# Kernel tuning notes

Measured on AMD Instinct MI355X. Metric: run time of the kernel, lower is better.

Reference implementation:

```python
import jax, jax.numpy as jnp
import numpy as np

D = 512      # model_dim
H = 8        # num_heads
HD = D // H  # head_dim = 64
S = 196      # tokens per channel (14x14 grid)
CHANNELS = np.array([2, 4, 6, 4], dtype=np.int32)  # multiplex channels per sample


def setup_inputs() -> dict:
    key = jax.random.key(0)
    ks = jax.random.split(key, 8)
    C = int(CHANNELS.sum())  # 16
    n = lambda k, shp, s=1.0: jax.random.normal(k, shp, dtype=jnp.float32) * s
    return {
        "x_query": n(ks[0], (C, S, D)),
        "x_keyval": n(ks[1], (C, S, D)),
        "pos": n(ks[2], (C, S, D)),
        "channels": CHANNELS,
        "Wq": n(ks[3], (D, D), 0.02), "bq": jnp.zeros((D,), jnp.float32),
        "Wk": n(ks[4], (D, D), 0.02), "bk": jnp.zeros((D,), jnp.float32),
        "Wv": n(ks[5], (D, D), 0.02), "bv": jnp.zeros((D,), jnp.float32),
        "Wo": n(ks[6], (D, D), 0.02), "bo": jnp.zeros((D,), jnp.float32),
    }


def reference(x_query, x_keyval, pos, channels, Wq, bq, Wk, bk, Wv, bv, Wo, bo):
    C, S_, D_ = x_query.shape
    ch = np.asarray(channels)
    # segment id per packed token; segment i has length channels[i]*S (== cu_seq_len blocks)
    seg = np.repeat(np.arange(ch.shape[0]), ch * S_)                # [T] static
    block_mask = seg[:, None] == seg[None, :]                        # [T,T] static bool

    xq = x_query.reshape(-1, D_)   # [T,D]
    xk = x_keyval.reshape(-1, D_)
    p = pos.reshape(-1, D_)

    # positional embedding fused into Q/K before projection (query_pos/key_pos)
    q = ((xq + p) @ Wq + bq).reshape(-1, H, HD)
    k = ((xk + p) @ Wk + bk).reshape(-1, H, HD)
    v = (xk @ Wv + bv).reshape(-1, H, HD)

    scale = 1.0 / np.sqrt(HD)
    scores = jnp.einsum('qhd,khd->hqk', q, k) * scale               # [H,T,T]
    scores = jnp.where(block_mask[None], scores, jnp.float32(-1e30))
    attn = jax.nn.softmax(scores, axis=-1)
    out = jnp.einsum('hqk,khd->qhd', attn, v).reshape(-1, D_)       # [T,D]
    out = out @ Wo + bo
    return out.reshape(C, S_, D_)
```

## Files before the change

### kernel.cpp

```cpp
#include <hip/hip_runtime.h>


typedef short short8 __attribute__((ext_vector_type(8)));
typedef float f32x4 __attribute__((ext_vector_type(4)));

__device__ __forceinline__ float b2f(unsigned short u) {
    union { float f; unsigned int i; } x; x.i = ((unsigned int)u) << 16; return x.f;
}
__device__ __forceinline__ unsigned short f2b(float f) {
    union { float f; unsigned int i; } x; x.f = f;
    unsigned int r = x.i + 0x7fffu + ((x.i >> 16) & 1u);
    return (unsigned short)(r >> 16);
}

#define NE 1605632
#define WE 262144
#define GS 72

__launch_bounds__(256)
__global__ void prep(const float* __restrict__ xq, const float* __restrict__ xk,
                     const float* __restrict__ pos,
                     const float* __restrict__ W0, const float* __restrict__ W1,
                     const float* __restrict__ W2, const float* __restrict__ W3,
                     unsigned short* __restrict__ WF,
                     unsigned short* __restrict__ aqb, unsigned short* __restrict__ akb,
                     unsigned short* __restrict__ xkbb) {
    const int tid = threadIdx.x;
    if (blockIdx.z < 4) {
        if (blockIdx.x >= 128) return;
        const float* W = blockIdx.z == 0 ? W0 : blockIdx.z == 1 ? W1 : blockIdx.z == 2 ? W2 : W3;
        unsigned short* T = WF + (size_t)blockIdx.z * WE;
        const int s = blockIdx.x * 4 + (tid >> 6);
        const int f = s >> 4, t = s & 15;
        const int lane = tid & 63, quad = lane >> 4, l16 = lane & 15;
        short8 o;
        #pragma unroll
        for (int j = 0; j < 8; ++j)
            o[j] = (short)f2b(W[(size_t)(t * 32 + quad * 8 + j) * 512 + f * 16 + l16]);
        *(short8*)(T + (size_t)s * 512 + lane * 8) = o;
    } else {
        const size_t e = ((size_t)blockIdx.x * 256 + tid) * 8;
        f32x4 q0 = *(const f32x4*)(xq + e),  q1 = *(const f32x4*)(xq + e + 4);
        f32x4 k0 = *(const f32x4*)(xk + e),  k1 = *(const f32x4*)(xk + e + 4);
        f32x4 p0 = *(const f32x4*)(pos + e), p1 = *(const f32x4*)(pos + e + 4);
        short8 a, b, c;
        #pragma unroll
        for (int j = 0; j < 4; ++j) {
            a[j] = (short)f2b(q0[j] + p0[j]); a[4 + j] = (short)f2b(q1[j] + p1[j]);
            b[j] = (short)f2b(k0[j] + p0[j]); b[4 + j] = (short)f2b(k1[j] + p1[j]);
            c[j] = (short)f2b(k0[j]);         c[4 + j] = (short)f2b(k1[j]);
        }
        *(short8*)(aqb + e)  = a;
        *(short8*)(akb + e)  = b;
        *(short8*)(xkbb + e) = c;
    }
}

template <bool OUT_F32>
__device__ __forceinline__ void gemm_wave(const unsigned short* __restrict__ A,
                                          const unsigned short* __restrict__ WFw,
                                          const float* __restrict__ bias,
                                          void* __restrict__ C,
                                          int m0, int n0) {
    const int lane = threadIdx.x & 63;
    const int quad = lane >> 4, l16 = lane & 15;
    const int f0 = n0 >> 4;
    const unsigned short* Arow = A + (size_t)(m0 + l16) * 512 + quad * 8;
    const unsigned short* Bbase = WFw + (size_t)lane * 8;

    f32x4 acc[4] = {};
    #pragma unroll 4
    for (int t = 0; t < 16; ++t) {
        short8 af = *(const short8*)(Arow + t * 32);
        #pragma unroll
        for (int nt = 0; nt < 4; ++nt) {
            short8 bf = *(const short8*)(Bbase + (size_t)((f0 + nt) * 16 + t) * 512);
            acc[nt] = __builtin_amdgcn_mfma_f32_16x16x32_bf16(af, bf, acc[nt], 0, 0, 0);
        }
    }
    #pragma unroll
    for (int nt = 0; nt < 4; ++nt) {
        const int col = n0 + nt * 16 + l16;
        const float bv = bias[col];
        #pragma unroll
        for (int r = 0; r < 4; ++r) {
            const int row = m0 + quad * 4 + r;
            float cv = acc[nt][r] + bv;
            if constexpr (OUT_F32) ((float*)C)[(size_t)row * 512 + col] = cv;
            else ((unsigned short*)C)[(size_t)row * 512 + col] = f2b(cv);
        }
    }
}

__launch_bounds__(256)
__global__ void qkv_gemm(const unsigned short* __restrict__ aqb,
                         const unsigned short* __restrict__ akb,
                         const unsigned short* __restrict__ xkbb,
                         const unsigned short* __restrict__ WF,
                         const float* __restrict__ bq, const float* __restrict__ bk,
                         const float* __restrict__ bv,
                         unsigned short* __restrict__ qb, unsigned short* __restrict__ kb,
                         unsigned short* __restrict__ vb) {
    const unsigned short* A; const unsigned short* WFw; const float* bias; unsigned short* C;
    switch (blockIdx.z) {
        case 0:  A = aqb;  WFw = WF;          bias = bq; C = qb; break;
        case 1:  A = akb;  WFw = WF + WE;     bias = bk; C = kb; break;
        default: A = xkbb; WFw = WF + 2 * WE; bias = bv; C = vb; break;
    }
    gemm_wave<false>(A, WFw, bias, C, blockIdx.x * 64 + (threadIdx.x >> 6) * 16,
                     blockIdx.y * 64);
}

__launch_bounds__(256)
__global__ void out_gemm(const unsigned short* __restrict__ A,
                         const unsigned short* __restrict__ WFo,
                         const float* __restrict__ bo, float* __restrict__ out) {
    gemm_wave<true>(A, WFo, bo, out, blockIdx.x * 64 + (threadIdx.x >> 6) * 16,
                    blockIdx.y * 64);
}

__launch_bounds__(256)
__global__ void attn_seg(const unsigned short* __restrict__ q,
                         const unsigned short* __restrict__ k,
                         const unsigned short* __restrict__ v,
                         unsigned short* __restrict__ o) {
    __shared__ __align__(16) unsigned short Ks[64 * GS];
    __shared__ __align__(16) unsigned short Vt[64 * GS];
    __shared__ __align__(16) unsigned short Pb[4][16 * GS];
    const int bx = blockIdx.x, h = blockIdx.y;
    int off, L, qt;
    if (bx < 7)       { off = 0;    L = 392;  qt = bx; }
    else if (bx < 20) { off = 392;  L = 784;  qt = bx - 7; }
    else if (bx < 39) { off = 1176; L = 1176; qt = bx - 20; }
    else              { off = 2352; L = 784;  qt = bx - 39; }
    const int tid = threadIdx.x;
    const int wave = tid >> 6, lane = tid & 63;
    const int quad = lane >> 4, l16 = lane & 15;
    const int hb = h * 64;
    const int lastr = off + L - 1;

    int qrow = off + qt * 64 + wave * 16 + l16;
    if (qrow > lastr) qrow = lastr;
    short8 aq0 = *(const short8*)(q + (size_t)qrow * 512 + hb + quad * 8);
    short8 aq1 = *(const short8*)(q + (size_t)qrow * 512 + hb + 32 + quad * 8);

    const int skey = tid & 63, sd = (tid >> 6) * 16;
    const int ntiles = (L + 63) >> 6;

    float lrow[4] = {0.f, 0.f, 0.f, 0.f};
    f32x4 oacc[4] = {};

    short8 kr0, kr1, vr0, vr1;
    {
        int krow = off + skey;
        kr0 = *(const short8*)(k + (size_t)krow * 512 + hb + sd);
        kr1 = *(const short8*)(k + (size_t)krow * 512 + hb + sd + 8);
        vr0 = *(const short8*)(v + (size_t)krow * 512 + hb + sd);
        vr1 = *(const short8*)(v + (size_t)krow * 512 + hb + sd + 8);
    }
    for (int b = 0; b < ntiles; ++b) {
        __syncthreads();
        *(short8*)(Ks + skey * GS + sd)     = kr0;
        *(short8*)(Ks + skey * GS + sd + 8) = kr1;
        #pragma unroll
        for (int j = 0; j < 8; ++j) {
            Vt[(sd + j) * GS + skey]     = (unsigned short)vr0[j];
            Vt[(sd + 8 + j) * GS + skey] = (unsigned short)vr1[j];
        }
        __syncthreads();
        if (b + 1 < ntiles) {
            int kk = (b + 1) * 64 + skey;
            int krow = off + (kk < L ? kk : L - 1);
            kr0 = *(const short8*)(k + (size_t)krow * 512 + hb + sd);
            kr1 = *(const short8*)(k + (size_t)krow * 512 + hb + sd + 8);
            vr0 = *(const short8*)(v + (size_t)krow * 512 + hb + sd);
            vr1 = *(const short8*)(v + (size_t)krow * 512 + hb + sd + 8);
        }
        f32x4 s[4];
        #pragma unroll
        for (int g = 0; g < 4; ++g) {
            short8 kb0 = *(const short8*)(Ks + (g * 16 + l16) * GS + quad * 8);
            short8 kb1 = *(const short8*)(Ks + (g * 16 + l16) * GS + 32 + quad * 8);
            f32x4 z = {0.f, 0.f, 0.f, 0.f};
            z = __builtin_amdgcn_mfma_f32_16x16x32_bf16(aq0, kb0, z, 0, 0, 0);
            s[g] = __builtin_amdgcn_mfma_f32_16x16x32_bf16(aq1, kb1, z, 0, 0, 0);
        }
        float p[4][4];
        #pragma unroll
        for (int g = 0; g < 4; ++g) {
            const bool valid = (b * 64 + g * 16 + l16) < L;
            #pragma unroll
            for (int r = 0; r < 4; ++r) {
                p[g][r] = valid ? __expf(fminf(s[g][r] * 0.125f, 30.f)) : 0.f;
                lrow[r] += p[g][r];
            }
        }
        #pragma unroll
        for (int g = 0; g < 4; ++g)
            #pragma unroll
            for (int r = 0; r < 4; ++r)
                Pb[wave][(quad * 4 + r) * GS + g * 16 + l16] = f2b(p[g][r]);
        short8 pa0 = *(const short8*)(Pb[wave] + l16 * GS + quad * 8);
        short8 pa1 = *(const short8*)(Pb[wave] + l16 * GS + 32 + quad * 8);
        #pragma unroll
        for (int nt = 0; nt < 4; ++nt) {
            short8 vf0 = *(const short8*)(Vt + (nt * 16 + l16) * GS + quad * 8);
            short8 vf1 = *(const short8*)(Vt + (nt * 16 + l16) * GS + 32 + quad * 8);
            oacc[nt] = __builtin_amdgcn_mfma_f32_16x16x32_bf16(pa0, vf0, oacc[nt], 0, 0, 0);
            oacc[nt] = __builtin_amdgcn_mfma_f32_16x16x32_bf16(pa1, vf1, oacc[nt], 0, 0, 0);
        }
    }
    #pragma unroll
    for (int r = 0; r < 4; ++r) {
        #pragma unroll
        for (int msk = 1; msk < 16; msk <<= 1)
            lrow[r] += __shfl_xor(lrow[r], msk);
    }
    float linv[4];
    #pragma unroll
    for (int r = 0; r < 4; ++r) linv[r] = 1.0f / lrow[r];
    #pragma unroll
    for (int nt = 0; nt < 4; ++nt) {
        #pragma unroll
        for (int r = 0; r < 4; ++r) {
            const int qi = qt * 64 + wave * 16 + quad * 4 + r;
            if (qi < L)
                o[(size_t)(off + qi) * 512 + hb + nt * 16 + l16] = f2b(oacc[nt][r] * linv[r]);
        }
    }
}

extern "C" void kernel_launch(void* const* d_in, const int* in_sizes, int n_in,
                              void* d_out, int out_size, void* d_ws, size_t ws_size,
                              hipStream_t stream) {
    const float* xq  = (const float*)d_in[0];
    const float* xk  = (const float*)d_in[1];
    const float* pos = (const float*)d_in[2];
    const float* Wq = (const float*)d_in[4];
    const float* bq = (const float*)d_in[5];
    const float* Wk = (const float*)d_in[6];
    const float* bk = (const float*)d_in[7];
    const float* Wv = (const float*)d_in[8];
    const float* bv = (const float*)d_in[9];
    const float* Wo = (const float*)d_in[10];
    const float* bo = (const float*)d_in[11];
    float* out = (float*)d_out;

    unsigned short* ws = (unsigned short*)d_ws;
    unsigned short* qb   = ws;
    unsigned short* kb   = ws + NE;
    unsigned short* vb   = ws + (size_t)2 * NE;
    unsigned short* aqb  = ws + (size_t)3 * NE;
    unsigned short* akb  = ws + (size_t)4 * NE;
    unsigned short* xkbb = ws + (size_t)5 * NE;
    unsigned short* WF   = ws + (size_t)6 * NE;

    prep<<<dim3(784, 1, 5), 256, 0, stream>>>(xq, xk, pos, Wq, Wk, Wv, Wo,
                                              WF, aqb, akb, xkbb);
    qkv_gemm<<<dim3(49, 8, 3), 256, 0, stream>>>(aqb, akb, xkbb, WF, bq, bk, bv,
                                                 qb, kb, vb);
    attn_seg<<<dim3(52, 8), 256, 0, stream>>>(qb, kb, vb, qb);
    out_gemm<<<dim3(49, 8), 256, 0, stream>>>(qb, WF + (size_t)3 * WE, bo, out);
}
```

Measured before the change: 153.0 us.

## Fuse activation bf16 conversion into QKV GEMM and split attention keys across waves

The prep kernel now converts only the weights. The pos add and bf16 conversion of activations move into the QKV GEMM's A-operand load, which removes three intermediate bf16 activation buffers and their write/read traffic. Attention now uses 32-row query tiles, with wave pairs splitting each 64-key tile and combining partial outputs and row sums through shared memory at the end. That doubles the number of blocks (100x8) for more occupancy on the GPU, at the cost of more K/V reloads per query row and a final shared-memory reduction. The fused GEMM also re-reads fp32 activations once per N tile, since the 8 column blocks each convert them again.

```diff
diff --git a/kernel.cpp b/kernel.cpp
--- a/kernel.cpp
+++ b/kernel.cpp
@@ -16,62 +16,55 @@
 #define NE 1605632
 #define WE 262144
 #define GS 72
-
-__launch_bounds__(256)
-__global__ void prep(const float* __restrict__ xq, const float* __restrict__ xk,
-                     const float* __restrict__ pos,
-                     const float* __restrict__ W0, const float* __restrict__ W1,
-                     const float* __restrict__ W2, const float* __restrict__ W3,
-                     unsigned short* __restrict__ WF,
-                     unsigned short* __restrict__ aqb, unsigned short* __restrict__ akb,
-                     unsigned short* __restrict__ xkbb) {
+#define PS 40
+#define OS 66
+
+__launch_bounds__(256)
+__global__ void prep_w(const float* __restrict__ W0, const float* __restrict__ W1,
+                       const float* __restrict__ W2, const float* __restrict__ W3,
+                       unsigned short* __restrict__ WF) {
     const int tid = threadIdx.x;
-    if (blockIdx.z < 4) {
-        if (blockIdx.x >= 128) return;
-        const float* W = blockIdx.z == 0 ? W0 : blockIdx.z == 1 ? W1 : blockIdx.z == 2 ? W2 : W3;
-        unsigned short* T = WF + (size_t)blockIdx.z * WE;
-        const int s = blockIdx.x * 4 + (tid >> 6);
-        const int f = s >> 4, t = s & 15;
-        const int lane = tid & 63, quad = lane >> 4, l16 = lane & 15;
-        short8 o;
-        #pragma unroll
-        for (int j = 0; j < 8; ++j)
-            o[j] = (short)f2b(W[(size_t)(t * 32 + quad * 8 + j) * 512 + f * 16 + l16]);
-        *(short8*)(T + (size_t)s * 512 + lane * 8) = o;
-    } else {
-        const size_t e = ((size_t)blockIdx.x * 256 + tid) * 8;
-        f32x4 q0 = *(const f32x4*)(xq + e),  q1 = *(const f32x4*)(xq + e + 4);
-        f32x4 k0 = *(const f32x4*)(xk + e),  k1 = *(const f32x4*)(xk + e + 4);
-        f32x4 p0 = *(const f32x4*)(pos + e), p1 = *(const f32x4*)(pos + e + 4);
-        short8 a, b, c;
-        #pragma unroll
-        for (int j = 0; j < 4; ++j) {
-            a[j] = (short)f2b(q0[j] + p0[j]); a[4 + j] = (short)f2b(q1[j] + p1[j]);
-            b[j] = (short)f2b(k0[j] + p0[j]); b[4 + j] = (short)f2b(k1[j] + p1[j]);
-            c[j] = (short)f2b(k0[j]);         c[4 + j] = (short)f2b(k1[j]);
-        }
-        *(short8*)(aqb + e)  = a;
-        *(short8*)(akb + e)  = b;
-        *(short8*)(xkbb + e) = c;
-    }
-}
-
-template <bool OUT_F32>
-__device__ __forceinline__ void gemm_wave(const unsigned short* __restrict__ A,
-                                          const unsigned short* __restrict__ WFw,
-                                          const float* __restrict__ bias,
-                                          void* __restrict__ C,
-                                          int m0, int n0) {
+    const int wjob = blockIdx.x * 4 + (tid >> 6);
+    const int w = wjob >> 9, s = wjob & 511;
+    const float* W = w == 0 ? W0 : w == 1 ? W1 : w == 2 ? W2 : W3;
+    unsigned short* T = WF + (size_t)w * WE;
+    const int f = s >> 4, t = s & 15;
+    const int lane = tid & 63, quad = lane >> 4, l16 = lane & 15;
+    short8 o;
+    #pragma unroll
+    for (int j = 0; j < 8; ++j)
+        o[j] = (short)f2b(W[(size_t)(t * 32 + quad * 8 + j) * 512 + f * 16 + l16]);
+    *(short8*)(T + (size_t)s * 512 + lane * 8) = o;
+}
+
+template <bool HAS_P>
+__device__ __forceinline__ void qkv_wave(const float* __restrict__ X,
+                                         const float* __restrict__ P,
+                                         const unsigned short* __restrict__ WFw,
+                                         const float* __restrict__ bias,
+                                         unsigned short* __restrict__ C,
+                                         int m0, int n0) {
     const int lane = threadIdx.x & 63;
     const int quad = lane >> 4, l16 = lane & 15;
     const int f0 = n0 >> 4;
-    const unsigned short* Arow = A + (size_t)(m0 + l16) * 512 + quad * 8;
+    const float* Xrow = X + (size_t)(m0 + l16) * 512 + quad * 8;
+    const float* Prow = HAS_P ? P + (size_t)(m0 + l16) * 512 + quad * 8 : nullptr;
     const unsigned short* Bbase = WFw + (size_t)lane * 8;
 
     f32x4 acc[4] = {};
     #pragma unroll 4
     for (int t = 0; t < 16; ++t) {
-        short8 af = *(const short8*)(Arow + t * 32);
+        f32x4 x0 = *(const f32x4*)(Xrow + t * 32);
+        f32x4 x1 = *(const f32x4*)(Xrow + t * 32 + 4);
+        if constexpr (HAS_P) {
+            f32x4 p0 = *(const f32x4*)(Prow + t * 32);
+            f32x4 p1 = *(const f32x4*)(Prow + t * 32 + 4);
+            #pragma unroll
+            for (int j = 0; j < 4; ++j) { x0[j] += p0[j]; x1[j] += p1[j]; }
+        }
+        short8 af;
+        #pragma unroll
+        for (int j = 0; j < 4; ++j) { af[j] = (short)f2b(x0[j]); af[4 + j] = (short)f2b(x1[j]); }
         #pragma unroll
         for (int nt = 0; nt < 4; ++nt) {
             short8 bf = *(const short8*)(Bbase + (size_t)((f0 + nt) * 16 + t) * 512);
@@ -85,61 +78,83 @@
         #pragma unroll
         for (int r = 0; r < 4; ++r) {
             const int row = m0 + quad * 4 + r;
-            float cv = acc[nt][r] + bv;
-            if constexpr (OUT_F32) ((float*)C)[(size_t)row * 512 + col] = cv;
-            else ((unsigned short*)C)[(size_t)row * 512 + col] = f2b(cv);
-        }
-    }
-}
-
-__launch_bounds__(256)
-__global__ void qkv_gemm(const unsigned short* __restrict__ aqb,
-                         const unsigned short* __restrict__ akb,
-                         const unsigned short* __restrict__ xkbb,
+            C[(size_t)row * 512 + col] = f2b(acc[nt][r] + bv);
+        }
+    }
+}
+
+__launch_bounds__(256)
+__global__ void qkv_gemm(const float* __restrict__ xq, const float* __restrict__ xk,
+                         const float* __restrict__ pos,
                          const unsigned short* __restrict__ WF,
                          const float* __restrict__ bq, const float* __restrict__ bk,
                          const float* __restrict__ bv,
                          unsigned short* __restrict__ qb, unsigned short* __restrict__ kb,
                          unsigned short* __restrict__ vb) {
-    const unsigned short* A; const unsigned short* WFw; const float* bias; unsigned short* C;
+    const int m0 = blockIdx.x * 64 + (threadIdx.x >> 6) * 16, n0 = blockIdx.y * 64;
     switch (blockIdx.z) {
-        case 0:  A = aqb;  WFw = WF;          bias = bq; C = qb; break;
-        case 1:  A = akb;  WFw = WF + WE;     bias = bk; C = kb; break;
-        default: A = xkbb; WFw = WF + 2 * WE; bias = bv; C = vb; break;
-    }
-    gemm_wave<false>(A, WFw, bias, C, blockIdx.x * 64 + (threadIdx.x >> 6) * 16,
-                     blockIdx.y * 64);
+        case 0:  qkv_wave<true >(xq, pos, WF,          bq, qb, m0, n0); break;
+        case 1:  qkv_wave<true >(xk, pos, WF + WE,     bk, kb, m0, n0); break;
+        default: qkv_wave<false>(xk, nullptr, WF + 2 * WE, bv, vb, m0, n0); break;
+    }
 }
 
 __launch_bounds__(256)
 __global__ void out_gemm(const unsigned short* __restrict__ A,
                          const unsigned short* __restrict__ WFo,
                          const float* __restrict__ bo, float* __restrict__ out) {
-    gemm_wave<true>(A, WFo, bo, out, blockIdx.x * 64 + (threadIdx.x >> 6) * 16,
-                    blockIdx.y * 64);
-}
-
-__launch_bounds__(256)
-__global__ void attn_seg(const unsigned short* __restrict__ q,
-                         const unsigned short* __restrict__ k,
-                         const unsigned short* __restrict__ v,
-                         unsigned short* __restrict__ o) {
+    const int lane = threadIdx.x & 63;
+    const int quad = lane >> 4, l16 = lane & 15;
+    const int m0 = blockIdx.x * 64 + (threadIdx.x >> 6) * 16, n0 = blockIdx.y * 64;
+    const int f0 = n0 >> 4;
+    const unsigned short* Arow = A + (size_t)(m0 + l16) * 512 + quad * 8;
+    const unsigned short* Bbase = WFo + (size_t)lane * 8;
+
+    f32x4 acc[4] = {};
+    #pragma unroll 4
+    for (int t = 0; t < 16; ++t) {
+        short8 af = *(const short8*)(Arow + t * 32);
+        #pragma unroll
+        for (int nt = 0; nt < 4; ++nt) {
+            short8 bf = *(const short8*)(Bbase + (size_t)((f0 + nt) * 16 + t) * 512);
+            acc[nt] = __builtin_amdgcn_mfma_f32_16x16x32_bf16(af, bf, acc[nt], 0, 0, 0);
+        }
+    }
+    #pragma unroll
+    for (int nt = 0; nt < 4; ++nt) {
+        const int col = n0 + nt * 16 + l16;
+        const float bv = bo[col];
+        #pragma unroll
+        for (int r = 0; r < 4; ++r)
+            out[(size_t)(m0 + quad * 4 + r) * 512 + col] = acc[nt][r] + bv;
+    }
+}
+
+__launch_bounds__(256)
+__global__ void attn32(const unsigned short* __restrict__ q,
+                       const unsigned short* __restrict__ k,
+                       const unsigned short* __restrict__ v,
+                       unsigned short* __restrict__ o) {
     __shared__ __align__(16) unsigned short Ks[64 * GS];
     __shared__ __align__(16) unsigned short Vt[64 * GS];
-    __shared__ __align__(16) unsigned short Pb[4][16 * GS];
+    __shared__ __align__(16) unsigned short Pb[4][16 * PS];
+    __shared__ float Obuf[2][16 * OS];
+    __shared__ float Lbuf[2][16];
     const int bx = blockIdx.x, h = blockIdx.y;
     int off, L, qt;
-    if (bx < 7)       { off = 0;    L = 392;  qt = bx; }
-    else if (bx < 20) { off = 392;  L = 784;  qt = bx - 7; }
-    else if (bx < 39) { off = 1176; L = 1176; qt = bx - 20; }
-    else              { off = 2352; L = 784;  qt = bx - 39; }
+    if (bx < 13)      { off = 0;    L = 392;  qt = bx; }
+    else if (bx < 38) { off = 392;  L = 784;  qt = bx - 13; }
+    else if (bx < 75) { off = 1176; L = 1176; qt = bx - 38; }
+    else              { off = 2352; L = 784;  qt = bx - 75; }
     const int tid = threadIdx.x;
     const int wave = tid >> 6, lane = tid & 63;
     const int quad = lane >> 4, l16 = lane & 15;
+    const int rw = wave & 1;
+    const int kh = (wave >> 1) * 32;
     const int hb = h * 64;
     const int lastr = off + L - 1;
 
-    int qrow = off + qt * 64 + wave * 16 + l16;
+    int qrow = off + qt * 32 + rw * 16 + l16;
     if (qrow > lastr) qrow = lastr;
     short8 aq0 = *(const short8*)(q + (size_t)qrow * 512 + hb + quad * 8);
     short8 aq1 = *(const short8*)(q + (size_t)qrow * 512 + hb + 32 + quad * 8);
@@ -176,19 +191,20 @@
             vr0 = *(const short8*)(v + (size_t)krow * 512 + hb + sd);
             vr1 = *(const short8*)(v + (size_t)krow * 512 + hb + sd + 8);
         }
-        f32x4 s[4];
-        #pragma unroll
-        for (int g = 0; g < 4; ++g) {
-            short8 kb0 = *(const short8*)(Ks + (g * 16 + l16) * GS + quad * 8);
-            short8 kb1 = *(const short8*)(Ks + (g * 16 + l16) * GS + 32 + quad * 8);
+        f32x4 s[2];
+        #pragma unroll
+        for (int g = 0; g < 2; ++g) {
+            const int kk = kh + g * 16 + l16;
+            short8 kb0 = *(const short8*)(Ks + kk * GS + quad * 8);
+            short8 kb1 = *(const short8*)(Ks + kk * GS + 32 + quad * 8);
             f32x4 z = {0.f, 0.f, 0.f, 0.f};
             z = __builtin_amdgcn_mfma_f32_16x16x32_bf16(aq0, kb0, z, 0, 0, 0);
             s[g] = __builtin_amdgcn_mfma_f32_16x16x32_bf16(aq1, kb1, z, 0, 0, 0);
         }
-        float p[4][4];
-        #pragma unroll
-        for (int g = 0; g < 4; ++g) {
-            const bool valid = (b * 64 + g * 16 + l16) < L;
+        float p[2][4];
+        #pragma unroll
+        for (int g = 0; g < 2; ++g) {
+            const bool valid = (b * 64 + kh + g * 16 + l16) < L;
             #pragma unroll
             for (int r = 0; r < 4; ++r) {
                 p[g][r] = valid ? __expf(fminf(s[g][r] * 0.125f, 30.f)) : 0.f;
@@ -196,18 +212,15 @@
             }
         }
         #pragma unroll
-        for (int g = 0; g < 4; ++g)
+        for (int g = 0; g < 2; ++g)
             #pragma unroll
             for (int r = 0; r < 4; ++r)
-                Pb[wave][(quad * 4 + r) * GS + g * 16 + l16] = f2b(p[g][r]);
-        short8 pa0 = *(const short8*)(Pb[wave] + l16 * GS + quad * 8);
-        short8 pa1 = *(const short8*)(Pb[wave] + l16 * GS + 32 + quad * 8);
-        #pragma unroll
-        for (int nt = 0; nt < 4; ++nt) {
-            short8 vf0 = *(const short8*)(Vt + (nt * 16 + l16) * GS + quad * 8);
-            short8 vf1 = *(const short8*)(Vt + (nt * 16 + l16) * GS + 32 + quad * 8);
-            oacc[nt] = __builtin_amdgcn_mfma_f32_16x16x32_bf16(pa0, vf0, oacc[nt], 0, 0, 0);
-            oacc[nt] = __builtin_amdgcn_mfma_f32_16x16x32_bf16(pa1, vf1, oacc[nt], 0, 0, 0);
+                Pb[wave][(quad * 4 + r) * PS + g * 16 + l16] = f2b(p[g][r]);
+        short8 pa = *(const short8*)(Pb[wave] + l16 * PS + quad * 8);
+        #pragma unroll
+        for (int nt = 0; nt < 4; ++nt) {
+            short8 vf = *(const short8*)(Vt + (nt * 16 + l16) * GS + kh + quad * 8);
+            oacc[nt] = __builtin_amdgcn_mfma_f32_16x16x32_bf16(pa, vf, oacc[nt], 0, 0, 0);
         }
     }
     #pragma unroll
@@ -216,16 +229,33 @@
         for (int msk = 1; msk < 16; msk <<= 1)
             lrow[r] += __shfl_xor(lrow[r], msk);
     }
-    float linv[4];
-    #pragma unroll
-    for (int r = 0; r < 4; ++r) linv[r] = 1.0f / lrow[r];
-    #pragma unroll
-    for (int nt = 0; nt < 4; ++nt) {
-        #pragma unroll
-        for (int r = 0; r < 4; ++r) {
-            const int qi = qt * 64 + wave * 16 + quad * 4 + r;
-            if (qi < L)
-                o[(size_t)(off + qi) * 512 + hb + nt * 16 + l16] = f2b(oacc[nt][r] * linv[r]);
+    if (wave >= 2) {
+        #pragma unroll
+        for (int nt = 0; nt < 4; ++nt)
+            #pragma unroll
+            for (int r = 0; r < 4; ++r)
+                Obuf[rw][(quad * 4 + r) * OS + nt * 16 + l16] = oacc[nt][r];
+        if (l16 == 0)
+            Lbuf[rw][quad * 4 + 0] = lrow[0], Lbuf[rw][quad * 4 + 1] = lrow[1],
+            Lbuf[rw][quad * 4 + 2] = lrow[2], Lbuf[rw][quad * 4 + 3] = lrow[3];
+    }
+    __syncthreads();
+    if (wave < 2) {
+        float linv[4];
+        #pragma unroll
+        for (int r = 0; r < 4; ++r)
+            linv[r] = 1.0f / (lrow[r] + Lbuf[rw][quad * 4 + r]);
+        #pragma unroll
+        for (int nt = 0; nt < 4; ++nt) {
+            #pragma unroll
+            for (int r = 0; r < 4; ++r) {
+                const int qi = qt * 32 + rw * 16 + quad * 4 + r;
+                if (qi < L) {
+                    float val = (oacc[nt][r] + Obuf[rw][(quad * 4 + r) * OS + nt * 16 + l16])
+                                * linv[r];
+                    o[(size_t)(off + qi) * 512 + hb + nt * 16 + l16] = f2b(val);
+                }
+            }
         }
     }
 }
@@ -247,18 +277,13 @@
     float* out = (float*)d_out;
 
     unsigned short* ws = (unsigned short*)d_ws;
-    unsigned short* qb   = ws;
-    unsigned short* kb   = ws + NE;
-    unsigned short* vb   = ws + (size_t)2 * NE;
-    unsigned short* aqb  = ws + (size_t)3 * NE;
-    unsigned short* akb  = ws + (size_t)4 * NE;
-    unsigned short* xkbb = ws + (size_t)5 * NE;
-    unsigned short* WF   = ws + (size_t)6 * NE;
-
-    prep<<<dim3(784, 1, 5), 256, 0, stream>>>(xq, xk, pos, Wq, Wk, Wv, Wo,
-                                              WF, aqb, akb, xkbb);
-    qkv_gemm<<<dim3(49, 8, 3), 256, 0, stream>>>(aqb, akb, xkbb, WF, bq, bk, bv,
-                                                 qb, kb, vb);
-    attn_seg<<<dim3(52, 8), 256, 0, stream>>>(qb, kb, vb, qb);
+    unsigned short* qb = ws;
+    unsigned short* kb = ws + NE;
+    unsigned short* vb = ws + (size_t)2 * NE;
+    unsigned short* WF = ws + (size_t)3 * NE;
+
+    prep_w<<<dim3(512), 256, 0, stream>>>(Wq, Wk, Wv, Wo, WF);
+    qkv_gemm<<<dim3(49, 8, 3), 256, 0, stream>>>(xq, xk, pos, WF, bq, bk, bv, qb, kb, vb);
+    attn32<<<dim3(100, 8), 256, 0, stream>>>(qb, kb, vb, qb);
     out_gemm<<<dim3(49, 8), 256, 0, stream>>>(qb, WF + (size_t)3 * WE, bo, out);
 }
```

Result: slower. 178.1 us (+16.4%).

## Split attention into 32-row query tiles with key-split waves and smem reduction

Applied to the files above, without the earlier changes.

Each attention block now handles 32 query rows instead of 64, which grows the grid from 52 to 100 blocks per head. Within a block, two wave pairs each take one half of every 64-key tile. The two partial outputs and row sums are merged through shared memory before normalisation. The goal is better CU occupancy and load balance on the GPU. The cost is that each K/V tile is reloaded by twice as many blocks, and the final merge adds an extra barrier.

```diff
diff --git a/kernel.cpp b/kernel.cpp
--- a/kernel.cpp
+++ b/kernel.cpp
@@ -16,6 +16,8 @@
 #define NE 1605632
 #define WE 262144
 #define GS 72
+#define PS 40
+#define OS 66
 
 __launch_bounds__(256)
 __global__ void prep(const float* __restrict__ xq, const float* __restrict__ xk,
@@ -120,26 +122,30 @@
 }
 
 __launch_bounds__(256)
-__global__ void attn_seg(const unsigned short* __restrict__ q,
-                         const unsigned short* __restrict__ k,
-                         const unsigned short* __restrict__ v,
-                         unsigned short* __restrict__ o) {
+__global__ void attn32(const unsigned short* __restrict__ q,
+                       const unsigned short* __restrict__ k,
+                       const unsigned short* __restrict__ v,
+                       unsigned short* __restrict__ o) {
     __shared__ __align__(16) unsigned short Ks[64 * GS];
     __shared__ __align__(16) unsigned short Vt[64 * GS];
-    __shared__ __align__(16) unsigned short Pb[4][16 * GS];
+    __shared__ __align__(16) unsigned short Pb[4][16 * PS];
+    __shared__ float Obuf[2][16 * OS];
+    __shared__ float Lbuf[2][16];
     const int bx = blockIdx.x, h = blockIdx.y;
     int off, L, qt;
-    if (bx < 7)       { off = 0;    L = 392;  qt = bx; }
-    else if (bx < 20) { off = 392;  L = 784;  qt = bx - 7; }
-    else if (bx < 39) { off = 1176; L = 1176; qt = bx - 20; }
-    else              { off = 2352; L = 784;  qt = bx - 39; }
+    if (bx < 13)      { off = 0;    L = 392;  qt = bx; }
+    else if (bx < 38) { off = 392;  L = 784;  qt = bx - 13; }
+    else if (bx < 75) { off = 1176; L = 1176; qt = bx - 38; }
+    else              { off = 2352; L = 784;  qt = bx - 75; }
     const int tid = threadIdx.x;
     const int wave = tid >> 6, lane = tid & 63;
     const int quad = lane >> 4, l16 = lane & 15;
+    const int rw = wave & 1;
+    const int kh = (wave >> 1) * 32;
     const int hb = h * 64;
     const int lastr = off + L - 1;
 
-    int qrow = off + qt * 64 + wave * 16 + l16;
+    int qrow = off + qt * 32 + rw * 16 + l16;
     if (qrow > lastr) qrow = lastr;
     short8 aq0 = *(const short8*)(q + (size_t)qrow * 512 + hb + quad * 8);
     short8 aq1 = *(const short8*)(q + (size_t)qrow * 512 + hb + 32 + quad * 8);
@@ -176,19 +182,20 @@
             vr0 = *(const short8*)(v + (size_t)krow * 512 + hb + sd);
             vr1 = *(const short8*)(v + (size_t)krow * 512 + hb + sd + 8);
         }
-        f32x4 s[4];
-        #pragma unroll
-        for (int g = 0; g < 4; ++g) {
-            short8 kb0 = *(const short8*)(Ks + (g * 16 + l16) * GS + quad * 8);
-            short8 kb1 = *(const short8*)(Ks + (g * 16 + l16) * GS + 32 + quad * 8);
+        f32x4 s[2];
+        #pragma unroll
+        for (int g = 0; g < 2; ++g) {
+            const int kk = kh + g * 16 + l16;
+            short8 kb0 = *(const short8*)(Ks + kk * GS + quad * 8);
+            short8 kb1 = *(const short8*)(Ks + kk * GS + 32 + quad * 8);
             f32x4 z = {0.f, 0.f, 0.f, 0.f};
             z = __builtin_amdgcn_mfma_f32_16x16x32_bf16(aq0, kb0, z, 0, 0, 0);
             s[g] = __builtin_amdgcn_mfma_f32_16x16x32_bf16(aq1, kb1, z, 0, 0, 0);
         }
-        float p[4][4];
-        #pragma unroll
-        for (int g = 0; g < 4; ++g) {
-            const bool valid = (b * 64 + g * 16 + l16) < L;
+        float p[2][4];
+        #pragma unroll
+        for (int g = 0; g < 2; ++g) {
+            const bool valid = (b * 64 + kh + g * 16 + l16) < L;
             #pragma unroll
             for (int r = 0; r < 4; ++r) {
                 p[g][r] = valid ? __expf(fminf(s[g][r] * 0.125f, 30.f)) : 0.f;
@@ -196,18 +203,15 @@
             }
         }
         #pragma unroll
-        for (int g = 0; g < 4; ++g)
+        for (int g = 0; g < 2; ++g)
             #pragma unroll
             for (int r = 0; r < 4; ++r)
-                Pb[wave][(quad * 4 + r) * GS + g * 16 + l16] = f2b(p[g][r]);
-        short8 pa0 = *(const short8*)(Pb[wave] + l16 * GS + quad * 8);
-        short8 pa1 = *(const short8*)(Pb[wave] + l16 * GS + 32 + quad * 8);
+                Pb[wave][(quad * 4 + r) * PS + g * 16 + l16] = f2b(p[g][r]);
+        short8 pa = *(const short8*)(Pb[wave] + l16 * PS + quad * 8);
         #pragma unroll
         for (int nt = 0; nt < 4; ++nt) {
-            short8 vf0 = *(const short8*)(Vt + (nt * 16 + l16) * GS + quad * 8);
-            short8 vf1 = *(const short8*)(Vt + (nt * 16 + l16) * GS + 32 + quad * 8);
-            oacc[nt] = __builtin_amdgcn_mfma_f32_16x16x32_bf16(pa0, vf0, oacc[nt], 0, 0, 0);
-            oacc[nt] = __builtin_amdgcn_mfma_f32_16x16x32_bf16(pa1, vf1, oacc[nt], 0, 0, 0);
+            short8 vf = *(const short8*)(Vt + (nt * 16 + l16) * GS + kh + quad * 8);
+            oacc[nt] = __builtin_amdgcn_mfma_f32_16x16x32_bf16(pa, vf, oacc[nt], 0, 0, 0);
         }
     }
     #pragma unroll
@@ -216,16 +220,34 @@
         for (int msk = 1; msk < 16; msk <<= 1)
             lrow[r] += __shfl_xor(lrow[r], msk);
     }
-    float linv[4];
-    #pragma unroll
-    for (int r = 0; r < 4; ++r) linv[r] = 1.0f / lrow[r];
-    #pragma unroll
-    for (int nt = 0; nt < 4; ++nt) {
-        #pragma unroll
-        for (int r = 0; r < 4; ++r) {
-            const int qi = qt * 64 + wave * 16 + quad * 4 + r;
-            if (qi < L)
-                o[(size_t)(off + qi) * 512 + hb + nt * 16 + l16] = f2b(oacc[nt][r] * linv[r]);
+    if (wave >= 2) {
+        #pragma unroll
+        for (int nt = 0; nt < 4; ++nt)
+            #pragma unroll
+            for (int r = 0; r < 4; ++r)
+                Obuf[rw][(quad * 4 + r) * OS + nt * 16 + l16] = oacc[nt][r];
+        if (l16 == 0) {
+            Lbuf[rw][quad * 4 + 0] = lrow[0]; Lbuf[rw][quad * 4 + 1] = lrow[1];
+            Lbuf[rw][quad * 4 + 2] = lrow[2]; Lbuf[rw][quad * 4 + 3] = lrow[3];
+        }
+    }
+    __syncthreads();
+    if (wave < 2) {
+        float linv[4];
+        #pragma unroll
+        for (int r = 0; r < 4; ++r)
+            linv[r] = 1.0f / (lrow[r] + Lbuf[rw][quad * 4 + r]);
+        #pragma unroll
+        for (int nt = 0; nt < 4; ++nt) {
+            #pragma unroll
+            for (int r = 0; r < 4; ++r) {
+                const int qi = qt * 32 + rw * 16 + quad * 4 + r;
+                if (qi < L) {
+                    float val = (oacc[nt][r] + Obuf[rw][(quad * 4 + r) * OS + nt * 16 + l16])
+                                * linv[r];
+                    o[(size_t)(off + qi) * 512 + hb + nt * 16 + l16] = f2b(val);
+                }
+            }
         }
     }
 }
@@ -259,6 +281,6 @@
                                               WF, aqb, akb, xkbb);
     qkv_gemm<<<dim3(49, 8, 3), 256, 0, stream>>>(aqb, akb, xkbb, WF, bq, bk, bv,
                                                  qb, kb, vb);
-    attn_seg<<<dim3(52, 8), 256, 0, stream>>>(qb, kb, vb, qb);
+    attn32<<<dim3(100, 8), 256, 0, stream>>>(qb, kb, vb, qb);
     out_gemm<<<dim3(49, 8), 256, 0, stream>>>(qb, WF + (size_t)3 * WE, bo, out);
 }
```

After: 155.3 us. Within noise of the previous version (+1.5%).

## Double-buffer K/V shared tiles in segmented attention and reorder blocks longest-first

Applied to the files above, without the earlier changes.

Attention now keeps two LDS buffers for the K and V tiles. The next tile is written after the current tile's compute, so each iteration needs one barrier instead of two. The block-to-segment map is reordered so the longest segment's query tiles launch first, which should balance the tail. The P staging buffer shrinks to a 32-column half and is filled and consumed in two halves; this adds redundant self-copy stores and an extra write/read round per tile, and it depends on wave-level ordering of the shared P writes.

```diff
diff --git a/kernel.cpp b/kernel.cpp
--- a/kernel.cpp
+++ b/kernel.cpp
@@ -16,6 +16,7 @@
 #define NE 1605632
 #define WE 262144
 #define GS 72
+#define PS 40
 
 __launch_bounds__(256)
 __global__ void prep(const float* __restrict__ xq, const float* __restrict__ xk,
@@ -124,15 +125,15 @@
                          const unsigned short* __restrict__ k,
                          const unsigned short* __restrict__ v,
                          unsigned short* __restrict__ o) {
-    __shared__ __align__(16) unsigned short Ks[64 * GS];
-    __shared__ __align__(16) unsigned short Vt[64 * GS];
-    __shared__ __align__(16) unsigned short Pb[4][16 * GS];
+    __shared__ __align__(16) unsigned short Ks[2][64 * GS];
+    __shared__ __align__(16) unsigned short Vt[2][64 * GS];
+    __shared__ __align__(16) unsigned short Pb[4][16 * PS];
     const int bx = blockIdx.x, h = blockIdx.y;
     int off, L, qt;
-    if (bx < 7)       { off = 0;    L = 392;  qt = bx; }
-    else if (bx < 20) { off = 392;  L = 784;  qt = bx - 7; }
-    else if (bx < 39) { off = 1176; L = 1176; qt = bx - 20; }
-    else              { off = 2352; L = 784;  qt = bx - 39; }
+    if (bx < 19)      { off = 1176; L = 1176; qt = bx; }
+    else if (bx < 32) { off = 392;  L = 784;  qt = bx - 19; }
+    else if (bx < 45) { off = 2352; L = 784;  qt = bx - 32; }
+    else              { off = 0;    L = 392;  qt = bx - 45; }
     const int tid = threadIdx.x;
     const int wave = tid >> 6, lane = tid & 63;
     const int quad = lane >> 4, l16 = lane & 15;
@@ -150,25 +151,27 @@
     float lrow[4] = {0.f, 0.f, 0.f, 0.f};
     f32x4 oacc[4] = {};
 
-    short8 kr0, kr1, vr0, vr1;
     {
         int krow = off + skey;
-        kr0 = *(const short8*)(k + (size_t)krow * 512 + hb + sd);
-        kr1 = *(const short8*)(k + (size_t)krow * 512 + hb + sd + 8);
-        vr0 = *(const short8*)(v + (size_t)krow * 512 + hb + sd);
-        vr1 = *(const short8*)(v + (size_t)krow * 512 + hb + sd + 8);
-    }
+        short8 kr0 = *(const short8*)(k + (size_t)krow * 512 + hb + sd);
+        short8 kr1 = *(const short8*)(k + (size_t)krow * 512 + hb + sd + 8);
+        short8 vr0 = *(const short8*)(v + (size_t)krow * 512 + hb + sd);
+        short8 vr1 = *(const short8*)(v + (size_t)krow * 512 + hb + sd + 8);
+        *(short8*)(Ks[0] + skey * GS + sd)     = kr0;
+        *(short8*)(Ks[0] + skey * GS + sd + 8) = kr1;
+        #pragma unroll
+        for (int j = 0; j < 8; ++j) {
+            Vt[0][(sd + j) * GS + skey]     = (unsigned short)vr0[j];
+            Vt[0][(sd + 8 + j) * GS + skey] = (unsigned short)vr1[j];
+        }
+    }
+    __syncthreads();
+
     for (int b = 0; b < ntiles; ++b) {
-        __syncthreads();
-        *(short8*)(Ks + skey * GS + sd)     = kr0;
-        *(short8*)(Ks + skey * GS + sd + 8) = kr1;
-        #pragma unroll
-        for (int j = 0; j < 8; ++j) {
-            Vt[(sd + j) * GS + skey]     = (unsigned short)vr0[j];
-            Vt[(sd + 8 + j) * GS + skey] = (unsigned short)vr1[j];
-        }
-        __syncthreads();
-        if (b + 1 < ntiles) {
+        const int cur = b & 1, nxt = cur ^ 1;
+        short8 kr0, kr1, vr0, vr1;
+        const bool more = (b + 1 < ntiles);
+        if (more) {
             int kk = (b + 1) * 64 + skey;
             int krow = off + (kk < L ? kk : L - 1);
             kr0 = *(const short8*)(k + (size_t)krow * 512 + hb + sd);
@@ -179,8 +182,8 @@
         f32x4 s[4];
         #pragma unroll
         for (int g = 0; g < 4; ++g) {
-            short8 kb0 = *(const short8*)(Ks + (g * 16 + l16) * GS + quad * 8);
-            short8 kb1 = *(const short8*)(Ks + (g * 16 + l16) * GS + 32 + quad * 8);
+            short8 kb0 = *(const short8*)(Ks[cur] + (g * 16 + l16) * GS + quad * 8);
+            short8 kb1 = *(const short8*)(Ks[cur] + (g * 16 + l16) * GS + 32 + quad * 8);
             f32x4 z = {0.f, 0.f, 0.f, 0.f};
             z = __builtin_amdgcn_mfma_f32_16x16x32_bf16(aq0, kb0, z, 0, 0, 0);
             s[g] = __builtin_amdgcn_mfma_f32_16x16x32_bf16(aq1, kb1, z, 0, 0, 0);
@@ -199,16 +202,37 @@
         for (int g = 0; g < 4; ++g)
             #pragma unroll
             for (int r = 0; r < 4; ++r)
-                Pb[wave][(quad * 4 + r) * GS + g * 16 + l16] = f2b(p[g][r]);
-        short8 pa0 = *(const short8*)(Pb[wave] + l16 * GS + quad * 8);
-        short8 pa1 = *(const short8*)(Pb[wave] + l16 * GS + 32 + quad * 8);
-        #pragma unroll
-        for (int nt = 0; nt < 4; ++nt) {
-            short8 vf0 = *(const short8*)(Vt + (nt * 16 + l16) * GS + quad * 8);
-            short8 vf1 = *(const short8*)(Vt + (nt * 16 + l16) * GS + 32 + quad * 8);
-            oacc[nt] = __builtin_amdgcn_mfma_f32_16x16x32_bf16(pa0, vf0, oacc[nt], 0, 0, 0);
-            oacc[nt] = __builtin_amdgcn_mfma_f32_16x16x32_bf16(pa1, vf1, oacc[nt], 0, 0, 0);
-        }
+                Pb[wave][(quad * 4 + r) * PS + (g & 1) * 16 + l16 + (g >> 1) * 16 * PS * 0] =
+                    f2b(p[g][r]);
+        #pragma unroll
+        for (int g = 2; g < 4; ++g)
+            #pragma unroll
+            for (int r = 0; r < 4; ++r)
+                Pb[wave][(quad * 4 + r) * PS + (g & 1) * 16 + l16] = Pb[wave][(quad * 4 + r) * PS + (g & 1) * 16 + l16];
+        #pragma unroll
+        for (int half = 0; half < 2; ++half) {
+            #pragma unroll
+            for (int g = 0; g < 2; ++g)
+                #pragma unroll
+                for (int r = 0; r < 4; ++r)
+                    Pb[wave][(quad * 4 + r) * PS + g * 16 + l16] = f2b(p[half * 2 + g][r]);
+            short8 pa = *(const short8*)(Pb[wave] + l16 * PS + quad * 8);
+            #pragma unroll
+            for (int nt = 0; nt < 4; ++nt) {
+                short8 vf = *(const short8*)(Vt[cur] + (nt * 16 + l16) * GS + half * 32 + quad * 8);
+                oacc[nt] = __builtin_amdgcn_mfma_f32_16x16x32_bf16(pa, vf, oacc[nt], 0, 0, 0);
+            }
+        }
+        if (more) {
+            *(short8*)(Ks[nxt] + skey * GS + sd)     = kr0;
+            *(short8*)(Ks[nxt] + skey * GS + sd + 8) = kr1;
+            #pragma unroll
+            for (int j = 0; j < 8; ++j) {
+                Vt[nxt][(sd + j) * GS + skey]     = (unsigned short)vr0[j];
+                Vt[nxt][(sd + 8 + j) * GS + skey] = (unsigned short)vr1[j];
+            }
+        }
+        __syncthreads();
     }
     #pragma unroll
     for (int r = 0; r < 4; ++r) {
```

Result: no change. 153.0 us (+0.0%).
